# Kernel optimization log

Measured on AMD Instinct MI355X. Metric: run time of the kernel, lower is better.

Reference implementation:

```python
import jax, jax.numpy as jnp
import numpy as np

N, T, E, A, D, O, S, R = 64, 1000, 512, 256, 256, 80, 64, 2
ATT_RANGE = 10
H = 4 * D  # LSTM hidden size = 1024
K = 31     # location conv kernel width


def setup_inputs() -> dict:
    key = jax.random.key(0)
    ks = jax.random.split(key, 16)
    def rn(k, shape, scale=0.05):
        return (jax.random.normal(k, shape) * scale).astype(jnp.float32)
    return {
        "input_enc": jax.random.normal(ks[0], (N, T, E), jnp.float32),
        "input_dec": jax.random.normal(ks[1], (N, O), jnp.float32),
        "spkr_vec": jax.random.normal(ks[2], (N, 1, S), jnp.float32),
        "lengths_enc": jnp.full((N,), T, dtype=jnp.int32),
        "w_enc": rn(ks[3], (E, A)), "b_enc": jnp.zeros((A,), jnp.float32),
        "w_spkr": rn(ks[4], (S, A)),
        "conv_w": rn(ks[5], (A, 1, K)),
        "w_proj": rn(ks[6], (A, 1)), "b_proj": jnp.zeros((1,), jnp.float32),
        "w_p1": rn(ks[7], (O + S, 2 * D)), "b_p1": jnp.zeros((2 * D,), jnp.float32),
        "w_p2": rn(ks[8], (2 * D, D)), "b_p2": jnp.zeros((D,), jnp.float32),
        "w_ih0": rn(ks[9], (E + D + S, 4 * H)), "w_hh0": rn(ks[10], (H, 4 * H)),
        "b_ih0": jnp.zeros((4 * H,), jnp.float32), "b_hh0": jnp.zeros((4 * H,), jnp.float32),
        "w_ih1": rn(ks[11], (H, 4 * H)), "w_hh1": rn(ks[12], (H, 4 * H)),
        "b_ih1": jnp.zeros((4 * H,), jnp.float32), "b_hh1": jnp.zeros((4 * H,), jnp.float32),
        "w_out": rn(ks[13], (E + H, O * R)), "b_out": jnp.zeros((O * R,), jnp.float32),
    }


def _softsign(x):
    return x / (1.0 + jnp.abs(x))


def _lstm_cell_zero_state(x, w_ih, b_ih, b_hh):
    # h0 = c0 = 0, so the w_hh contribution vanishes on the first step
    gates = x @ w_ih + b_ih + b_hh          # [N, 4H]
    i, f, g, o = jnp.split(gates, 4, axis=-1)  # torch gate order i,f,g,o
    c = jax.nn.sigmoid(i) * jnp.tanh(g)
    return jax.nn.sigmoid(o) * jnp.tanh(c)


def reference(input_enc, input_dec, spkr_vec, lengths_enc,
              w_enc, b_enc, w_spkr, conv_w, w_proj, b_proj,
              w_p1, b_p1, w_p2, b_p2,
              w_ih0, w_hh0, b_ih0, b_hh0, w_ih1, w_hh1, b_ih1, b_hh1,
              w_out, b_out):
    n, t_enc, _ = input_enc.shape
    # initial attention weights: one-hot at t=0 (null_state branch)
    a0 = jnp.zeros((n, t_enc), input_enc.dtype).at[:, 0].set(1.0)

    bias_enc = _softsign(input_enc @ w_enc + b_enc)   # [N, T, A]
    bias_spkr = _softsign(spkr_vec @ w_spkr)          # [N, 1, A] broadcast

    # location features: conv1d over prev attention, padding 15, no bias
    prev_feat = jax.lax.conv_general_dilated(
        a0[:, None, :], conv_w, (1,), [(K // 2, K // 2)],
        dimension_numbers=("NCH", "OIH", "NCH"))    # [N, A, T]
    prev_feat = prev_feat.transpose(0, 2, 1)          # [N, T, A]

    # hidden is None on the first step -> in_att_dec = 0
    e = bias_enc + bias_spkr + prev_feat              # [N, T, A]

    # windowed attention mask around argmax of previous weights (no grad)
    max_idx = jnp.argmax(a0, axis=1)                  # [N]
    lim = jnp.maximum(lengths_enc.astype(jnp.int32) - 1, 0)  # [N]
    offs = jnp.arange(ATT_RANGE, dtype=jnp.int32)
    idx1 = jnp.minimum(jnp.maximum(max_idx[:, None] + offs, 0), lim[:, None])
    idx2 = jnp.minimum(jnp.maximum(max_idx[:, None] - offs, 0), lim[:, None])
    idxs = jnp.concatenate([idx1, idx2], axis=1)      # [N, 2*ATT_RANGE]
    rows = jnp.arange(n)[:, None]
    att_mask = jnp.zeros((n, t_enc), e.dtype).at[rows, idxs].set(1.0)
    att_mask = jax.lax.stop_gradient(att_mask)

    logit = (jnp.tanh(e) @ w_proj + b_proj)[..., 0]   # [N, T]
    logit = logit - jnp.max(logit, axis=1, keepdims=True)
    w = jnp.exp(logit) * att_mask
    att = w / jnp.maximum(jnp.sum(w, axis=1, keepdims=True), 1e-12)  # F.normalize p=1

    context = jnp.einsum("nt,nte->ne", att, input_enc)  # [N, E]

    # prenet (dropout in eval mode = identity)
    spkr = spkr_vec[:, 0, :]
    pre = jnp.concatenate([input_dec, spkr], axis=-1)
    pre = jax.nn.relu(pre @ w_p1 + b_p1)
    pre = jax.nn.relu(pre @ w_p2 + b_p2)               # [N, D]

    x = jnp.concatenate([pre, context, spkr], axis=-1)  # [N, D+E+S]
    h1 = _lstm_cell_zero_state(x, w_ih0, b_ih0, b_hh0)   # [N, H]
    h2 = _lstm_cell_zero_state(h1, w_ih1, b_ih1, b_hh1)  # [N, H]
    _ = (w_hh0, w_hh1)  # recurrent weights unused on first step (zero state)

    dec = jnp.concatenate([h2, context], axis=-1)        # [N, H+E]
    out = (dec @ w_out + b_out).reshape(n, R, O)         # [N, r_factor, O]
    return out
```

## Files before the change

### kernel.cpp

```cpp
#include <hip/hip_runtime.h>
#include <hip/hip_bf16.h>
#include <math.h>

#define N_   64
#define T_   1000
#define E_   512
#define A_   256
#define O_   80
#define S_   64
#define H_   1024
#define G4_  4096
#define KC_  31

__device__ __forceinline__ float sigmoidf_(float x) { return 1.f / (1.f + __expf(-x)); }
__device__ __forceinline__ float softsignf_(float x) { return x / (1.f + fabsf(x)); }

__global__ __launch_bounds__(512) void logits_kernel(
    const float* __restrict__ enc,
    const float* __restrict__ spkr,
    const float* __restrict__ w_enc,
    const float* __restrict__ b_enc,
    const float* __restrict__ w_spkr,
    const float* __restrict__ conv_w,
    const float* __restrict__ w_proj,
    float* __restrict__ part) {
  int n  = blockIdx.x;
  int aq = blockIdx.y;
  int tid = threadIdx.x;
  int al = tid & 63;
  int kw = tid >> 6;
  int a  = aq * 64 + al;

  __shared__ float smem[5120];
  __shared__ float sp[S_];
  __shared__ float bsl[S_];

  if (tid < S_) sp[tid] = spkr[n * S_ + tid];
  {
    const float4* src = (const float4*)(enc + (size_t)n * T_ * E_);
    float4* dst = (float4*)smem;
    for (int i = tid; i < 1280; i += 512) dst[i] = src[i];
  }
  __syncthreads();

  if (tid < S_) {
    float b = 0.f;
    #pragma unroll 8
    for (int s = 0; s < S_; ++s) b += sp[s] * w_spkr[s * A_ + aq * 64 + tid];
    bsl[tid] = softsignf_(b);
  }

  float acc[10];
  #pragma unroll
  for (int t = 0; t < 10; ++t) acc[t] = 0.f;
  const int kbase = kw * 64;
  const float* wcol = w_enc + a;
  #pragma unroll 8
  for (int k = 0; k < 64; ++k) {
    float we = wcol[(size_t)(kbase + k) * A_];
    #pragma unroll
    for (int t = 0; t < 10; ++t)
      acc[t] = fmaf(smem[t * E_ + kbase + k], we, acc[t]);
  }

  __syncthreads();
  #pragma unroll
  for (int t = 0; t < 10; ++t) smem[(kw * 10 + t) * 64 + al] = acc[t];
  __syncthreads();

  #pragma unroll
  for (int tb = 0; tb < 10; tb += 8) {
    int t = tb + kw;
    if (t < 10 && (tb == 0 || kw < 2)) {
      float p = b_enc[a];
      #pragma unroll
      for (int w = 0; w < 8; ++w) p += smem[(w * 10 + t) * 64 + al];
      float e = softsignf_(p) + bsl[al] + conv_w[a * KC_ + (15 - t)];
      float l = tanhf(e) * w_proj[a];
      #pragma unroll
      for (int off = 32; off > 0; off >>= 1) l += __shfl_down(l, off);
      if (al == 0) part[(n * 10 + t) * 4 + aq] = l;
    }
  }
}

__global__ __launch_bounds__(512) void ctx_prenet_kernel(
    const float* __restrict__ enc,
    const float* __restrict__ dec_in,
    const float* __restrict__ spkr,
    const int*   __restrict__ lengths,
    const float* __restrict__ part,
    const float* __restrict__ w_p1,
    const float* __restrict__ b_p1,
    const float* __restrict__ w_p2,
    const float* __restrict__ b_p2,
    float* __restrict__ xbuf) {
  int n = blockIdx.x;
  int tid = threadIdx.x;
  __shared__ float att[10];
  __shared__ float incat[O_ + S_];
  __shared__ float pre1[512];
  __shared__ float pp2[2][A_];

  if (tid < S_) {
    float s = spkr[n * S_ + tid];
    incat[O_ + tid] = s;
    xbuf[n * 832 + 768 + tid] = s;
  }
  if (tid < O_) incat[tid] = dec_in[n * O_ + tid];
  if (tid == 0) {
    int lim = lengths[n] - 1; if (lim < 0) lim = 0;
    int tmax = lim < 9 ? lim : 9;
    float lg[10];
    float m = -1e30f;
    for (int t = 0; t <= tmax; ++t) {
      const float* p = &part[(n * 10 + t) * 4];
      lg[t] = p[0] + p[1] + p[2] + p[3];
      m = fmaxf(m, lg[t]);
    }
    float ssum = 0.f;
    for (int t = 0; t <= tmax; ++t) { float w = __expf(lg[t] - m); att[t] = w; ssum += w; }
    float inv = 1.f / fmaxf(ssum, 1e-12f);
    for (int t = 0; t <= tmax; ++t) att[t] *= inv;
    for (int t = tmax + 1; t < 10; ++t) att[t] = 0.f;
  }
  __syncthreads();

  {
    float c = 0.f;
    #pragma unroll
    for (int t = 0; t < 10; ++t)
      c = fmaf(att[t], enc[(size_t)n * T_ * E_ + t * E_ + tid], c);
    xbuf[n * 832 + 256 + tid] = c;
  }

  {
    float v = b_p1[tid];
    #pragma unroll 8
    for (int k = 0; k < O_ + S_; ++k) v = fmaf(incat[k], w_p1[k * 512 + tid], v);
    pre1[tid] = fmaxf(v, 0.f);
  }
  __syncthreads();

  {
    int c  = tid & 255;
    int kh = tid >> 8;
    float v = 0.f;
    #pragma unroll 8
    for (int k = kh * 256; k < kh * 256 + 256; ++k)
      v = fmaf(pre1[k], w_p2[k * A_ + c], v);
    pp2[kh][c] = v;
  }
  __syncthreads();
  if (tid < A_) {
    float v = b_p2[tid] + pp2[0][tid] + pp2[1][tid];
    xbuf[n * 832 + tid] = fmaxf(v, 0.f);
  }
}

__global__ void gemm_gates_kernel(const float* __restrict__ X, int ldx, int K,
                                  const float* __restrict__ W,
                                  const float* __restrict__ b1,
                                  const float* __restrict__ b2,
                                  float* __restrict__ G) {
  int bt = blockIdx.x;
  int c0 = bt * 16; if (c0 >= 1024) c0 += 1024;
  int tid = threadIdx.x;
  int tr = tid >> 4;
  int tc = tid & 15;

  __shared__ __align__(16) float xs[32][64];
  __shared__ __align__(16) float wst[16][36];

  float acc0 = 0.f, acc1 = 0.f, acc2 = 0.f, acc3 = 0.f;

  for (int k0 = 0; k0 < K; k0 += 32) {
    {
      int r  = tid >> 2;
      int kb = (tid & 3) * 8;
      const float* src = X + r * ldx + k0 + kb;
      float4 v0 = *(const float4*)(src);
      float4 v1 = *(const float4*)(src + 4);
      xs[kb + 0][r] = v0.x; xs[kb + 1][r] = v0.y; xs[kb + 2][r] = v0.z; xs[kb + 3][r] = v0.w;
      xs[kb + 4][r] = v1.x; xs[kb + 5][r] = v1.y; xs[kb + 6][r] = v1.z; xs[kb + 7][r] = v1.w;
    }
    {
      int kk = tid >> 4;
      int c  = tid & 15;
      wst[c][kk]      = W[(size_t)(k0 + kk)      * G4_ + c0 + c];
      wst[c][kk + 16] = W[(size_t)(k0 + kk + 16) * G4_ + c0 + c];
    }
    __syncthreads();
    #pragma unroll
    for (int kq = 0; kq < 8; ++kq) {
      float4 wv = *(const float4*)&wst[tc][kq * 4];
      float4 x0 = *(const float4*)&xs[kq * 4 + 0][tr * 4];
      acc0 = fmaf(x0.x, wv.x, acc0); acc1 = fmaf(x0.y, wv.x, acc1);
      acc2 = fmaf(x0.z, wv.x, acc2); acc3 = fmaf(x0.w, wv.x, acc3);
      float4 x1 = *(const float4*)&xs[kq * 4 + 1][tr * 4];
      acc0 = fmaf(x1.x, wv.y, acc0); acc1 = fmaf(x1.y, wv.y, acc1);
      acc2 = fmaf(x1.z, wv.y, acc2); acc3 = fmaf(x1.w, wv.y, acc3);
      float4 x2 = *(const float4*)&xs[kq * 4 + 2][tr * 4];
      acc0 = fmaf(x2.x, wv.z, acc0); acc1 = fmaf(x2.y, wv.z, acc1);
      acc2 = fmaf(x2.z, wv.z, acc2); acc3 = fmaf(x2.w, wv.z, acc3);
      float4 x3 = *(const float4*)&xs[kq * 4 + 3][tr * 4];
      acc0 = fmaf(x3.x, wv.w, acc0); acc1 = fmaf(x3.y, wv.w, acc1);
      acc2 = fmaf(x3.z, wv.w, acc2); acc3 = fmaf(x3.w, wv.w, acc3);
    }
    __syncthreads();
  }

  int c = c0 + tc;
  float bb = b1[c] + b2[c];
  int r = tr * 4;
  G[(size_t)(r + 0) * G4_ + c] = acc0 + bb;
  G[(size_t)(r + 1) * G4_ + c] = acc1 + bb;
  G[(size_t)(r + 2) * G4_ + c] = acc2 + bb;
  G[(size_t)(r + 3) * G4_ + c] = acc3 + bb;
}

__global__ void lstm_act_kernel(const float* __restrict__ G, float* __restrict__ H) {
  int n = blockIdx.x;
  int tid = threadIdx.x;
  for (int j = tid; j < H_; j += 256) {
    float gi = G[(size_t)n * G4_ + j];
    float gg = G[(size_t)n * G4_ + 2048 + j];
    float go = G[(size_t)n * G4_ + 3072 + j];
    float cc = sigmoidf_(gi) * tanhf(gg);
    H[n * H_ + j] = sigmoidf_(go) * tanhf(cc);
  }
}

__global__ __launch_bounds__(1024) void out_kernel(
    const float* __restrict__ G1,
    const float* __restrict__ xbuf,
    const float* __restrict__ w_out,
    const float* __restrict__ b_out,
    float* __restrict__ out) {
  int n = blockIdx.x;
  int tid = threadIdx.x;
  __shared__ float dl[1536];
  __shared__ float pp[6][160];
  {
    float gi = G1[(size_t)n * G4_ + tid];
    float gg = G1[(size_t)n * G4_ + 2048 + tid];
    float go = G1[(size_t)n * G4_ + 3072 + tid];
    dl[tid] = sigmoidf_(go) * tanhf(sigmoidf_(gi) * tanhf(gg));
  }
  if (tid < E_) dl[1024 + tid] = xbuf[n * 832 + 256 + tid];
  __syncthreads();
  if (tid < 960) {
    int c  = tid % 160;
    int kq = tid / 160;
    float acc = 0.f;
    const float* wp = w_out + (size_t)(kq * 256) * 160 + c;
    const float* dp = dl + kq * 256;
    #pragma unroll 8
    for (int k = 0; k < 256; ++k) acc = fmaf(dp[k], wp[(size_t)k * 160], acc);
    pp[kq][c] = acc;
  }
  __syncthreads();
  if (tid < 160) {
    float r = b_out[tid] + pp[0][tid] + pp[1][tid] + pp[2][tid]
            + pp[3][tid] + pp[4][tid] + pp[5][tid];
    out[n * 160 + tid] = r;
  }
}

extern "C" void kernel_launch(void* const* d_in, const int* in_sizes, int n_in,
                              void* d_out, int out_size, void* d_ws, size_t ws_size,
                              hipStream_t stream) {
  const float* input_enc = (const float*)d_in[0];
  const float* input_dec = (const float*)d_in[1];
  const float* spkr_vec  = (const float*)d_in[2];
  const int*   lengths   = (const int*)  d_in[3];
  const float* w_enc     = (const float*)d_in[4];
  const float* b_enc     = (const float*)d_in[5];
  const float* w_spkr    = (const float*)d_in[6];
  const float* conv_w    = (const float*)d_in[7];
  const float* w_proj    = (const float*)d_in[8];
  const float* w_p1      = (const float*)d_in[10];
  const float* b_p1      = (const float*)d_in[11];
  const float* w_p2      = (const float*)d_in[12];
  const float* b_p2      = (const float*)d_in[13];
  const float* w_ih0     = (const float*)d_in[14];
  const float* b_ih0     = (const float*)d_in[16];
  const float* b_hh0     = (const float*)d_in[17];
  const float* w_ih1     = (const float*)d_in[18];
  const float* b_ih1     = (const float*)d_in[20];
  const float* b_hh1     = (const float*)d_in[21];
  const float* w_out     = (const float*)d_in[22];
  const float* b_out     = (const float*)d_in[23];

  float* ws    = (float*)d_ws;
  float* part  = ws;
  float* xbuf  = ws + 4096;
  float* gates = ws + 65536;
  float* h1    = ws + 327680;
  float* out   = (float*)d_out;

  hipLaunchKernelGGL(logits_kernel, dim3(64, 4), dim3(512), 0, stream,
                     input_enc, spkr_vec, w_enc, b_enc, w_spkr, conv_w, w_proj, part);
  hipLaunchKernelGGL(ctx_prenet_kernel, dim3(64), dim3(512), 0, stream,
                     input_enc, input_dec, spkr_vec, lengths, part,
                     w_p1, b_p1, w_p2, b_p2, xbuf);
  hipLaunchKernelGGL(gemm_gates_kernel, dim3(192), dim3(256), 0, stream,
                     xbuf, 832, 832, w_ih0, b_ih0, b_hh0, gates);
  hipLaunchKernelGGL(lstm_act_kernel, dim3(64), dim3(256), 0, stream, gates, h1);
  hipLaunchKernelGGL(gemm_gates_kernel, dim3(192), dim3(256), 0, stream,
                     h1, 1024, 1024, w_ih1, b_ih1, b_hh1, gates);
  hipLaunchKernelGGL(out_kernel, dim3(64), dim3(1024), 0, stream,
                     gates, xbuf, w_out, b_out, out);
}
```

Baseline: 107.4 us.

## Split-K gate GEMM with register-held weights and double-buffered X tiles

The gate GEMM now runs 512 threads per block, splitting K into two halves that are reduced through shared memory at the end. Weights are loaded straight into registers instead of staging through shared memory, and X tiles are double-buffered so the next chunk's global load overlaps the current FMAs, with one barrier per chunk. The LSTM activation kernel is flattened to one element per thread over 256 blocks. This adds register pressure (32 weight registers) and requires K/2 to be a multiple of 32, which holds for 832 and 1024.

```diff
diff --git a/kernel.cpp b/kernel.cpp
--- a/kernel.cpp
+++ b/kernel.cpp
@@ -158,77 +158,95 @@
   }
 }
 
-__global__ void gemm_gates_kernel(const float* __restrict__ X, int ldx, int K,
-                                  const float* __restrict__ W,
-                                  const float* __restrict__ b1,
-                                  const float* __restrict__ b2,
-                                  float* __restrict__ G) {
+__global__ __launch_bounds__(512) void gemm_gates_kernel(
+    const float* __restrict__ X, int ldx, int K,
+    const float* __restrict__ W,
+    const float* __restrict__ b1,
+    const float* __restrict__ b2,
+    float* __restrict__ G) {
   int bt = blockIdx.x;
   int c0 = bt * 16; if (c0 >= 1024) c0 += 1024;
   int tid = threadIdx.x;
-  int tr = tid >> 4;
-  int tc = tid & 15;
-
-  __shared__ __align__(16) float xs[32][64];
-  __shared__ __align__(16) float wst[16][36];
+  int kh  = tid >> 8;
+  int lt  = tid & 255;
+  int tr  = lt >> 4;
+  int tc  = lt & 15;
+  int c   = c0 + tc;
+  int Kh  = K >> 1;
+  int kbeg = kh * Kh;
+  int NC  = Kh >> 5;
+
+  int rr  = lt & 63;
+  int kb8 = (lt >> 6) << 3;
+
+  __shared__ float xs[2][2][32][64];
+  __shared__ float red[16][16][4];
+
+  const float* xsrc = X + (size_t)rr * ldx + kbeg + kb8;
+
+  float4 xv0 = ((const float4*)xsrc)[0];
+  float4 xv1 = ((const float4*)(xsrc + 4))[0];
+  {
+    float* d = &xs[kh][0][kb8][rr];
+    d[0]   = xv0.x; d[64]  = xv0.y; d[128] = xv0.z; d[192] = xv0.w;
+    d[256] = xv1.x; d[320] = xv1.y; d[384] = xv1.z; d[448] = xv1.w;
+  }
+  __syncthreads();
 
   float acc0 = 0.f, acc1 = 0.f, acc2 = 0.f, acc3 = 0.f;
-
-  for (int k0 = 0; k0 < K; k0 += 32) {
-    {
-      int r  = tid >> 2;
-      int kb = (tid & 3) * 8;
-      const float* src = X + r * ldx + k0 + kb;
-      float4 v0 = *(const float4*)(src);
-      float4 v1 = *(const float4*)(src + 4);
-      xs[kb + 0][r] = v0.x; xs[kb + 1][r] = v0.y; xs[kb + 2][r] = v0.z; xs[kb + 3][r] = v0.w;
-      xs[kb + 4][r] = v1.x; xs[kb + 5][r] = v1.y; xs[kb + 6][r] = v1.z; xs[kb + 7][r] = v1.w;
-    }
-    {
-      int kk = tid >> 4;
-      int c  = tid & 15;
-      wst[c][kk]      = W[(size_t)(k0 + kk)      * G4_ + c0 + c];
-      wst[c][kk + 16] = W[(size_t)(k0 + kk + 16) * G4_ + c0 + c];
+  for (int ch = 0; ch < NC; ++ch) {
+    int buf = ch & 1;
+    float wreg[32];
+    const float* wp = W + (size_t)(kbeg + ch * 32) * G4_ + c;
+    #pragma unroll
+    for (int kk = 0; kk < 32; ++kk) wreg[kk] = wp[(size_t)kk * G4_];
+    bool more = (ch + 1 < NC);
+    if (more) {
+      const float* s = xsrc + (ch + 1) * 32;
+      xv0 = ((const float4*)s)[0];
+      xv1 = ((const float4*)(s + 4))[0];
+    }
+    const float* xb = &xs[kh][buf][0][tr * 4];
+    #pragma unroll
+    for (int kk = 0; kk < 32; ++kk) {
+      float4 xv = *(const float4*)(xb + kk * 64);
+      acc0 = fmaf(xv.x, wreg[kk], acc0);
+      acc1 = fmaf(xv.y, wreg[kk], acc1);
+      acc2 = fmaf(xv.z, wreg[kk], acc2);
+      acc3 = fmaf(xv.w, wreg[kk], acc3);
+    }
+    if (more) {
+      float* d = &xs[kh][buf ^ 1][kb8][rr];
+      d[0]   = xv0.x; d[64]  = xv0.y; d[128] = xv0.z; d[192] = xv0.w;
+      d[256] = xv1.x; d[320] = xv1.y; d[384] = xv1.z; d[448] = xv1.w;
     }
     __syncthreads();
-    #pragma unroll
-    for (int kq = 0; kq < 8; ++kq) {
-      float4 wv = *(const float4*)&wst[tc][kq * 4];
-      float4 x0 = *(const float4*)&xs[kq * 4 + 0][tr * 4];
-      acc0 = fmaf(x0.x, wv.x, acc0); acc1 = fmaf(x0.y, wv.x, acc1);
-      acc2 = fmaf(x0.z, wv.x, acc2); acc3 = fmaf(x0.w, wv.x, acc3);
-      float4 x1 = *(const float4*)&xs[kq * 4 + 1][tr * 4];
-      acc0 = fmaf(x1.x, wv.y, acc0); acc1 = fmaf(x1.y, wv.y, acc1);
-      acc2 = fmaf(x1.z, wv.y, acc2); acc3 = fmaf(x1.w, wv.y, acc3);
-      float4 x2 = *(const float4*)&xs[kq * 4 + 2][tr * 4];
-      acc0 = fmaf(x2.x, wv.z, acc0); acc1 = fmaf(x2.y, wv.z, acc1);
-      acc2 = fmaf(x2.z, wv.z, acc2); acc3 = fmaf(x2.w, wv.z, acc3);
-      float4 x3 = *(const float4*)&xs[kq * 4 + 3][tr * 4];
-      acc0 = fmaf(x3.x, wv.w, acc0); acc1 = fmaf(x3.y, wv.w, acc1);
-      acc2 = fmaf(x3.z, wv.w, acc2); acc3 = fmaf(x3.w, wv.w, acc3);
-    }
-    __syncthreads();
-  }
-
-  int c = c0 + tc;
-  float bb = b1[c] + b2[c];
-  int r = tr * 4;
-  G[(size_t)(r + 0) * G4_ + c] = acc0 + bb;
-  G[(size_t)(r + 1) * G4_ + c] = acc1 + bb;
-  G[(size_t)(r + 2) * G4_ + c] = acc2 + bb;
-  G[(size_t)(r + 3) * G4_ + c] = acc3 + bb;
+  }
+
+  if (kh == 1) {
+    red[tr][tc][0] = acc0; red[tr][tc][1] = acc1;
+    red[tr][tc][2] = acc2; red[tr][tc][3] = acc3;
+  }
+  __syncthreads();
+  if (kh == 0) {
+    float bb = b1[c] + b2[c];
+    int r = tr * 4;
+    G[(size_t)(r + 0) * G4_ + c] = acc0 + red[tr][tc][0] + bb;
+    G[(size_t)(r + 1) * G4_ + c] = acc1 + red[tr][tc][1] + bb;
+    G[(size_t)(r + 2) * G4_ + c] = acc2 + red[tr][tc][2] + bb;
+    G[(size_t)(r + 3) * G4_ + c] = acc3 + red[tr][tc][3] + bb;
+  }
 }
 
 __global__ void lstm_act_kernel(const float* __restrict__ G, float* __restrict__ H) {
-  int n = blockIdx.x;
-  int tid = threadIdx.x;
-  for (int j = tid; j < H_; j += 256) {
-    float gi = G[(size_t)n * G4_ + j];
-    float gg = G[(size_t)n * G4_ + 2048 + j];
-    float go = G[(size_t)n * G4_ + 3072 + j];
-    float cc = sigmoidf_(gi) * tanhf(gg);
-    H[n * H_ + j] = sigmoidf_(go) * tanhf(cc);
-  }
+  int idx = blockIdx.x * 256 + threadIdx.x;
+  int n = idx >> 10;
+  int j = idx & 1023;
+  float gi = G[(size_t)n * G4_ + j];
+  float gg = G[(size_t)n * G4_ + 2048 + j];
+  float go = G[(size_t)n * G4_ + 3072 + j];
+  float cc = sigmoidf_(gi) * tanhf(gg);
+  H[n * H_ + j] = sigmoidf_(go) * tanhf(cc);
 }
 
 __global__ __launch_bounds__(1024) void out_kernel(
@@ -304,10 +322,10 @@
   hipLaunchKernelGGL(ctx_prenet_kernel, dim3(64), dim3(512), 0, stream,
                      input_enc, input_dec, spkr_vec, lengths, part,
                      w_p1, b_p1, w_p2, b_p2, xbuf);
-  hipLaunchKernelGGL(gemm_gates_kernel, dim3(192), dim3(256), 0, stream,
+  hipLaunchKernelGGL(gemm_gates_kernel, dim3(192), dim3(512), 0, stream,
                      xbuf, 832, 832, w_ih0, b_ih0, b_hh0, gates);
-  hipLaunchKernelGGL(lstm_act_kernel, dim3(64), dim3(256), 0, stream, gates, h1);
-  hipLaunchKernelGGL(gemm_gates_kernel, dim3(192), dim3(256), 0, stream,
+  hipLaunchKernelGGL(lstm_act_kernel, dim3(256), dim3(256), 0, stream, gates, h1);
+  hipLaunchKernelGGL(gemm_gates_kernel, dim3(192), dim3(512), 0, stream,
                      h1, 1024, 1024, w_ih1, b_ih1, b_hh1, gates);
   hipLaunchKernelGGL(out_kernel, dim3(64), dim3(1024), 0, stream,
                      gates, xbuf, w_out, b_out, out);
```

New measurement: 98.70 us, median of 2. 1.09x faster.
